# Performance work log

Hardware: AMD Instinct MI355X
Metric: run time of the kernel (lower is better)

Reference implementation:

```python
import jax, jax.numpy as jnp
import numpy as np

B, C_IN, C_OUT, N, K = 32, 16, 32, 2048, 3


def setup_inputs() -> dict:
    key = jax.random.key(0)
    k1, k2 = jax.random.split(key, 2)
    x = jax.random.normal(k1, (B, C_IN, N), dtype=jnp.float32)
    # Conv1d weight (out_channels, in_channels, K), Kaiming-ish scale
    W = jax.random.normal(k2, (C_OUT, C_IN, K), dtype=jnp.float32) * (1.0 / np.sqrt(C_IN * K))
    b = jnp.zeros((C_OUT,), dtype=jnp.float32)
    return {"x": x, "W": W, "b": b}


def reference(x, W, b):
    # x: (B, C, N) -- tokens are the N column vectors in channel space
    Bd, C, Nd = x.shape
    Kd = W.shape[2]
    # NNT: pairwise squared Euclidean distances between token vectors
    sq = jnp.sum(x * x, axis=1)                      # (B, N)
    gram = jnp.einsum('bcn,bcm->bnm', x, x)          # (B, N, N)
    dist = sq[:, :, None] - 2.0 * gram + sq[:, None, :]  # (B, N, N)
    # K nearest neighbors (smallest distance; self included at dist ~0)
    _, idx = jax.lax.top_k(-dist, Kd)                # (B, N, K) int32
    flat_idx = idx.reshape(Bd, Nd * Kd)              # (B, N*K)
    # gather neighbor columns -> prime: (B, C, N*K)
    prime = jnp.take_along_axis(x, flat_idx[:, None, :], axis=2)
    # Conv1d(kernel=K, stride=K) == per-group contraction over the K neighbors
    prime4 = prime.reshape(Bd, C, Nd, Kd)            # (B, C, N, K)
    out = jnp.einsum('bcnk,ock->bon', prime4, W) + b[None, :, None]
    return out  # (B, C_out, N)
```

## Files before the change

### kernel.cpp

```cpp
#include <hip/hip_runtime.h>
#include <float.h>
#include <limits.h>

#define BATCH 32
#define C_IN 16
#define C_OUT 32
#define NTOK 2048
#define KNN 3
#define ZH 2
#define MSEG (NTOK / ZH)
#define WPB 4
#define NPLANE 32

using f32x4v = __attribute__((ext_vector_type(4))) float;
using bf16x8 = __attribute__((ext_vector_type(8))) short;

__device__ __forceinline__ unsigned short f2bf(float f) {
    unsigned u = __float_as_uint(f);
    unsigned r = u + 0x7fffu + ((u >> 16) & 1u);
    return (unsigned short)(r >> 16);
}
__device__ __forceinline__ float bf2f(unsigned short h) {
    return __uint_as_float(((unsigned)h) << 16);
}
__device__ __forceinline__ unsigned umin2(unsigned a, unsigned b) { return a < b ? a : b; }
__device__ __forceinline__ unsigned med3u(unsigned a, unsigned b, unsigned c) {
    unsigned d;
    asm("v_med3_u32 %0, %1, %2, %3" : "=v"(d) : "v"(a), "v"(b), "v"(c));
    return d;
}

__global__ void __launch_bounds__(256) prep_kernel(
    const float* __restrict__ x, float* __restrict__ xTf,
    float* __restrict__ sqf, uint4* __restrict__ Am)
{
    const int n = blockIdx.x * 256 + threadIdx.x;
    const int b = blockIdx.y;
    const float* xb = x + (size_t)b * C_IN * NTOK;

    float v[C_IN];
#pragma unroll
    for (int c = 0; c < C_IN; ++c) v[c] = xb[(size_t)c * NTOK + n];

    float acc = 0.0f;
#pragma unroll
    for (int c = 0; c < C_IN; ++c) acc = __fadd_rn(acc, __fmul_rn(v[c], v[c]));
    sqf[(size_t)b * NTOK + n] = acc;

    float4* dst = (float4*)(xTf + ((size_t)b * NTOK + n) * C_IN);
#pragma unroll
    for (int j = 0; j < 4; ++j)
        dst[j] = make_float4(v[4*j+0], v[4*j+1], v[4*j+2], v[4*j+3]);

    unsigned hw[8], lw[8];
#pragma unroll
    for (int j = 0; j < 8; ++j) {
        const unsigned short h0 = f2bf(v[2*j]),   h1 = f2bf(v[2*j+1]);
        const unsigned short l0 = f2bf(v[2*j]   - bf2f(h0));
        const unsigned short l1 = f2bf(v[2*j+1] - bf2f(h1));
        hw[j] = (unsigned)h0 | ((unsigned)h1 << 16);
        lw[j] = (unsigned)l0 | ((unsigned)l1 << 16);
    }
    uint4* amb = Am + (size_t)b * NTOK * 4;
    const int nt  = n >> 4;
    const int col = n & 15;
    amb[nt*64 + 0*16 + col] = make_uint4(hw[0], hw[1], hw[2], hw[3]);
    amb[nt*64 + 1*16 + col] = make_uint4(hw[4], hw[5], hw[6], hw[7]);
    amb[nt*64 + 2*16 + col] = make_uint4(lw[0], lw[1], lw[2], lw[3]);
    amb[nt*64 + 3*16 + col] = make_uint4(lw[4], lw[5], lw[6], lw[7]);
}

__global__ void __launch_bounds__(256) knn_scan_kernel(
    const uint4* __restrict__ Am, const float* __restrict__ sqf,
    unsigned* __restrict__ keyws)
{
    const int tid  = threadIdx.x;
    const int w    = tid >> 6;
    const int l    = tid & 63;
    const int col  = l & 15;
    const int quad = l >> 4;

    const int wg   = blockIdx.x;
    const int b_lo = wg & 7;
    const int t2   = wg >> 3;
    const int b_hi = t2 >> 6;
    const int rest = t2 & 63;
    const int z    = rest >> 5;
    const int ntb  = rest & 31;
    const int b    = b_lo + (b_hi << 3);
    const int nt   = ntb * WPB + w;

    const int n  = nt * 16 + col;
    const int mbase = z * MSEG;

    const uint4* amb = Am + (size_t)b * NTOK * 4;
    const float* sqb = sqf + (size_t)b * NTOK;

    const uint4 bh4 = amb[(size_t)nt*64 + ((quad & 1) * 16) + col];
    const uint4 bl4 = amb[(size_t)nt*64 + ((2 + (quad & 1)) * 16) + col];
    const bf16x8 Bhi = *(const bf16x8*)&bh4;
    const bf16x8 Blo = *(const bf16x8*)&bl4;

    const float bias = sqb[n] + 4.0f;

    unsigned k0 = ~0u, k1 = ~0u, k2 = ~0u, k3 = ~0u;
    const int moff = quad * 4;
    const int tgbase = z * (MSEG / 16);

#pragma unroll 2
    for (int t = 0; t < MSEG / 16; ++t) {
        const uint4 af4 = amb[(size_t)(tgbase + t) * 64 + l];
        const bf16x8 Af = *(const bf16x8*)&af4;
        const float4 sq4 = *(const float4*)(sqb + mbase + t * 16 + moff);

        f32x4v acc = {0.0f, 0.0f, 0.0f, 0.0f};
        acc = __builtin_amdgcn_mfma_f32_16x16x32_bf16(Af, Bhi, acc, 0, 0, 0);
        acc = __builtin_amdgcn_mfma_f32_16x16x32_bf16(Af, Blo, acc, 0, 0, 0);

        const int mb = mbase + t * 16 + moff;
        const float sqa[4] = { sq4.x, sq4.y, sq4.z, sq4.w };
#pragma unroll
        for (int r = 0; r < 4; ++r) {
            const float d = __fadd_rn(__fmaf_rn(-2.0f, acc[r], sqa[r]), bias);
            const unsigned key = (__float_as_uint(d) & 0xFFFFF800u) | (unsigned)(mb + r);
            const unsigned ok0 = k0, ok1 = k1, ok2 = k2;
            k0 = umin2(key, k0);
            k1 = med3u(key, ok0, k1);
            k2 = med3u(key, ok1, k2);
            k3 = med3u(key, ok2, k3);
        }
    }

    const size_t plane = (size_t)BATCH * NTOK;
    unsigned* kp = keyws + ((size_t)((z * 4 + quad) * 4) * BATCH + b) * NTOK + n;
    kp[0]         = k0;
    kp[plane]     = k1;
    kp[2 * plane] = k2;
    kp[3 * plane] = k3;
}

__global__ void __launch_bounds__(256) rescore_conv_kernel(
    const float* __restrict__ xTf, const float* __restrict__ sqf,
    const unsigned* __restrict__ keyws, const float* __restrict__ W,
    const float* __restrict__ bias, float* __restrict__ out)
{
    const int wg   = blockIdx.x;
    const int b_lo = wg & 7;
    const int t2   = wg >> 3;
    const int b_hi = t2 >> 3;
    const int xc   = t2 & 7;
    const int b    = b_lo + (b_hi << 3);
    const int n    = xc * 256 + threadIdx.x;

    const float* sqb = sqf + (size_t)b * NTOK;
    const float* xb  = xTf + (size_t)b * NTOK * C_IN;

    float xn[C_IN];
    {
        const float4* src = (const float4*)(xb + (size_t)n * C_IN);
#pragma unroll
        for (int j = 0; j < 4; ++j) {
            const float4 tq = src[j];
            xn[4*j+0] = tq.x; xn[4*j+1] = tq.y; xn[4*j+2] = tq.z; xn[4*j+3] = tq.w;
        }
    }
    const float sqn = sqb[n];

    float D0 = FLT_MAX, D1 = FLT_MAX, D2 = FLT_MAX;
    int   I0 = INT_MAX, I1 = INT_MAX, I2 = INT_MAX;
    const size_t plane = (size_t)BATCH * NTOK;
    const size_t kbase = (size_t)b * NTOK + n;

#pragma unroll 4
    for (int p = 0; p < NPLANE; ++p) {
        const unsigned key = keyws[kbase + (size_t)p * plane];
        const int mi = (int)(key & 2047u);

        const float4* xm4 = (const float4*)(xb + (size_t)mi * C_IN);
        const float4 q0 = xm4[0], q1 = xm4[1], q2 = xm4[2], q3 = xm4[3];
        float g = 0.0f;
        g = __fmaf_rn(xn[0],  q0.x, g); g = __fmaf_rn(xn[1],  q0.y, g);
        g = __fmaf_rn(xn[2],  q0.z, g); g = __fmaf_rn(xn[3],  q0.w, g);
        g = __fmaf_rn(xn[4],  q1.x, g); g = __fmaf_rn(xn[5],  q1.y, g);
        g = __fmaf_rn(xn[6],  q1.z, g); g = __fmaf_rn(xn[7],  q1.w, g);
        g = __fmaf_rn(xn[8],  q2.x, g); g = __fmaf_rn(xn[9],  q2.y, g);
        g = __fmaf_rn(xn[10], q2.z, g); g = __fmaf_rn(xn[11], q2.w, g);
        g = __fmaf_rn(xn[12], q3.x, g); g = __fmaf_rn(xn[13], q3.y, g);
        g = __fmaf_rn(xn[14], q3.z, g); g = __fmaf_rn(xn[15], q3.w, g);
        const float d = __fadd_rn(__fmaf_rn(-2.0f, g, sqn), sqb[mi]);

        const bool c0 = (d < D0) || (d == D0 && mi < I0);
        const bool c1 = (d < D1) || (d == D1 && mi < I1);
        const bool c2 = (d < D2) || (d == D2 && mi < I2);
        const float oD0 = D0, oD1 = D1;
        const int   oI0 = I0, oI1 = I1;
        D0 = c0 ? d : D0;               I0 = c0 ? mi : I0;
        D1 = c0 ? oD0 : (c1 ? d : D1);  I1 = c0 ? oI0 : (c1 ? mi : I1);
        D2 = c1 ? oD1 : (c2 ? d : D2);  I2 = c1 ? oI1 : (c2 ? mi : I2);
    }

    float xg[KNN][C_IN];
    const int idx[KNN] = { I0, I1, I2 };
#pragma unroll
    for (int k = 0; k < KNN; ++k) {
        const float4* src = (const float4*)(xb + (size_t)idx[k] * C_IN);
#pragma unroll
        for (int j = 0; j < 4; ++j) {
            const float4 t = src[j];
            xg[k][4*j+0] = t.x; xg[k][4*j+1] = t.y;
            xg[k][4*j+2] = t.z; xg[k][4*j+3] = t.w;
        }
    }

#pragma unroll
    for (int o = 0; o < C_OUT; ++o) {
        float acc = bias[o];
#pragma unroll
        for (int c = 0; c < C_IN; ++c) {
#pragma unroll
            for (int k = 0; k < KNN; ++k)
                acc = __fmaf_rn(W[(o * C_IN + c) * KNN + k], xg[k][c], acc);
        }
        out[((size_t)b * C_OUT + o) * NTOK + n] = acc;
    }
}

extern "C" void kernel_launch(void* const* d_in, const int* in_sizes, int n_in,
                              void* d_out, int out_size, void* d_ws, size_t ws_size,
                              hipStream_t stream) {
    const float* x    = (const float*)d_in[0];
    const float* W    = (const float*)d_in[1];
    const float* bias = (const float*)d_in[2];
    float* out = (float*)d_out;

    char* ws = (char*)d_ws;
    const size_t BN = (size_t)BATCH * NTOK;
    uint4*    Am    = (uint4*)ws;
    float*    sqf   = (float*)(ws + BN * 64);
    float*    xTf   = (float*)(ws + BN * 68);
    unsigned* keyws = (unsigned*)(ws + BN * 68 + BN * 64);

    dim3 grid1(NTOK / 256, BATCH);
    prep_kernel<<<grid1, 256, 0, stream>>>(x, xTf, sqf, Am);

    knn_scan_kernel<<<dim3(BATCH * (NTOK / (16 * WPB)) * ZH), 256, 0, stream>>>(Am, sqf, keyws);

    rescore_conv_kernel<<<dim3(BATCH * (NTOK / 256)), 256, 0, stream>>>(xTf, sqf, keyws, W, bias, out);
}
```

Baseline: 77.14 us.

## Split rescore candidate planes and conv outputs across four waves per token group

The rescore kernel now gives each block 64 tokens and has its four wavefronts each rescore 8 of the 32 candidate planes. Partial top-3 lists are merged through LDS by the first wave, and the final indices are broadcast back through LDS. Each wave then computes a quarter of the output channels. This raises the block count fourfold and cuts the serial per-thread loop length, at the cost of two barriers, redundant loads of the token vector and its neighbours in every wave, and a serialized merge step.

```diff
diff --git a/kernel.cpp b/kernel.cpp
--- a/kernel.cpp
+++ b/kernel.cpp
@@ -144,13 +144,21 @@
     const unsigned* __restrict__ keyws, const float* __restrict__ W,
     const float* __restrict__ bias, float* __restrict__ out)
 {
+    __shared__ float lds_d[4][3][64];
+    __shared__ int   lds_i[4][3][64];
+    __shared__ int   lds_idx[3][64];
+
+    const int tid     = threadIdx.x;
+    const int psub    = tid >> 6;
+    const int n_local = tid & 63;
+
     const int wg   = blockIdx.x;
     const int b_lo = wg & 7;
     const int t2   = wg >> 3;
-    const int b_hi = t2 >> 3;
-    const int xc   = t2 & 7;
+    const int b_hi = t2 >> 5;
+    const int nc   = t2 & 31;
     const int b    = b_lo + (b_hi << 3);
-    const int n    = xc * 256 + threadIdx.x;
+    const int n    = nc * 64 + n_local;
 
     const float* sqb = sqf + (size_t)b * NTOK;
     const float* xb  = xTf + (size_t)b * NTOK * C_IN;
@@ -169,10 +177,10 @@
     float D0 = FLT_MAX, D1 = FLT_MAX, D2 = FLT_MAX;
     int   I0 = INT_MAX, I1 = INT_MAX, I2 = INT_MAX;
     const size_t plane = (size_t)BATCH * NTOK;
-    const size_t kbase = (size_t)b * NTOK + n;
+    const size_t kbase = (size_t)b * NTOK + n + (size_t)(psub * 8) * plane;
 
 #pragma unroll 4
-    for (int p = 0; p < NPLANE; ++p) {
+    for (int p = 0; p < 8; ++p) {
         const unsigned key = keyws[kbase + (size_t)p * plane];
         const int mi = (int)(key & 2047u);
 
@@ -199,8 +207,36 @@
         D2 = c1 ? oD1 : (c2 ? d : D2);  I2 = c1 ? oI1 : (c2 ? mi : I2);
     }
 
+    lds_d[psub][0][n_local] = D0;  lds_i[psub][0][n_local] = I0;
+    lds_d[psub][1][n_local] = D1;  lds_i[psub][1][n_local] = I1;
+    lds_d[psub][2][n_local] = D2;  lds_i[psub][2][n_local] = I2;
+    __syncthreads();
+
+    if (psub == 0) {
+#pragma unroll
+        for (int s = 1; s < 4; ++s) {
+#pragma unroll
+            for (int k = 0; k < KNN; ++k) {
+                const float d  = lds_d[s][k][n_local];
+                const int   mi = lds_i[s][k][n_local];
+                const bool c0 = (d < D0) || (d == D0 && mi < I0);
+                const bool c1 = (d < D1) || (d == D1 && mi < I1);
+                const bool c2 = (d < D2) || (d == D2 && mi < I2);
+                const float oD0 = D0, oD1 = D1;
+                const int   oI0 = I0, oI1 = I1;
+                D0 = c0 ? d : D0;               I0 = c0 ? mi : I0;
+                D1 = c0 ? oD0 : (c1 ? d : D1);  I1 = c0 ? oI0 : (c1 ? mi : I1);
+                D2 = c1 ? oD1 : (c2 ? d : D2);  I2 = c1 ? oI1 : (c2 ? mi : I2);
+            }
+        }
+        lds_idx[0][n_local] = I0;
+        lds_idx[1][n_local] = I1;
+        lds_idx[2][n_local] = I2;
+    }
+    __syncthreads();
+
+    const int idx[KNN] = { lds_idx[0][n_local], lds_idx[1][n_local], lds_idx[2][n_local] };
     float xg[KNN][C_IN];
-    const int idx[KNN] = { I0, I1, I2 };
 #pragma unroll
     for (int k = 0; k < KNN; ++k) {
         const float4* src = (const float4*)(xb + (size_t)idx[k] * C_IN);
@@ -213,7 +249,8 @@
     }
 
 #pragma unroll
-    for (int o = 0; o < C_OUT; ++o) {
+    for (int oo = 0; oo < C_OUT / 4; ++oo) {
+        const int o = psub * (C_OUT / 4) + oo;
         float acc = bias[o];
 #pragma unroll
         for (int c = 0; c < C_IN; ++c) {
@@ -245,5 +282,5 @@
 
     knn_scan_kernel<<<dim3(BATCH * (NTOK / (16 * WPB)) * ZH), 256, 0, stream>>>(Am, sqf, keyws);
 
-    rescore_conv_kernel<<<dim3(BATCH * (NTOK / 256)), 256, 0, stream>>>(xTf, sqf, keyws, W, bias, out);
-}
+    rescore_conv_kernel<<<dim3(BATCH * (NTOK / 64)), 256, 0, stream>>>(xTf, sqf, keyws, W, bias, out);
+}
```

After: 77.45 us. About the same (+0.4%).
